# Kernel optimization log

Measured on AMD Instinct MI355X. Metric: run time of the kernel, lower is better.

## Reference

```python
import jax, jax.numpy as jnp
import numpy as np

B, T, IN, H = 256, 512, 130, 512


def setup_inputs() -> dict:
    key = jax.random.key(0)
    ks = jax.random.split(key, 6)
    scale = 1.0 / np.sqrt(H)
    inputs = jax.random.normal(ks[0], (B, T, IN), dtype=jnp.float32)
    inputs_len = jax.random.randint(ks[1], (B,), 1, T + 1)
    h0 = jnp.zeros((B, H), dtype=jnp.float32)
    c0 = jnp.zeros((B, H), dtype=jnp.float32)
    W_ih = jax.random.normal(ks[2], (4 * H, IN - 2), dtype=jnp.float32) * scale
    W_hh = jax.random.normal(ks[3], (4 * H, H), dtype=jnp.float32) * scale
    b_ih = jax.random.normal(ks[4], (4 * H,), dtype=jnp.float32) * scale
    b_hh = jax.random.normal(ks[5], (4 * H,), dtype=jnp.float32) * scale
    return {"inputs": inputs, "inputs_len": inputs_len, "h0": h0, "c0": c0,
            "W_ih": W_ih, "W_hh": W_hh, "b_ih": b_ih, "b_hh": b_hh}


def reference(inputs, inputs_len, h0, c0, W_ih, W_hh, b_ih, b_hh):
    # stard_LSTM=True: drop last 2 input features (spatial coords)
    xs = jnp.transpose(inputs[:, :, :-2], (1, 0, 2))  # [T, B, IN-2]

    def step(carry, x_t):
        h, c = carry
        gates = x_t @ W_ih.T + b_ih + h @ W_hh.T + b_hh  # [B, 4H]
        i, f, g, o = jnp.split(gates, 4, axis=-1)  # torch LSTMCell gate order
        i = jax.nn.sigmoid(i)
        f = jax.nn.sigmoid(f)
        g = jnp.tanh(g)
        o = jax.nn.sigmoid(o)
        c = f * c + i * g
        h = o * jnp.tanh(c)
        return (h, c), h

    _, hs = jax.lax.scan(step, (h0, c0), xs)  # hs: [T, B, H]
    # gather last valid hidden state per sequence (outputs[len-1][b])
    batch_idx = jnp.arange(inputs.shape[0])
    return hs[inputs_len - 1, batch_idx]  # [B, H]
```

## Files before the change

### kernel.cpp

```cpp
#include <hip/hip_runtime.h>
#include <hip/hip_bf16.h>
#include <stdint.h>


#define NB 256
#define NT 512
#define NF 130
#define NK 128
#define NH 512

typedef float f32x4 __attribute__((ext_vector_type(4)));
typedef float f32x2 __attribute__((ext_vector_type(2)));
typedef short bf16x8 __attribute__((ext_vector_type(8)));

__device__ __forceinline__ short bf1(float f) {
  union { float f; uint32_t u; } v; v.f = f;
  uint32_t r = (v.u + 0x7FFFu + ((v.u >> 16) & 1u)) >> 16;
  return (short)r;
}

__device__ __forceinline__ bf16x8 cvt8(const float* p) {
  bf16x8 r;
#pragma unroll
  for (int i = 0; i < 4; ++i) {
    f32x2 t = *(const f32x2*)(p + 2 * i);
    r[2 * i]     = bf1(t[0]);
    r[2 * i + 1] = bf1(t[1]);
  }
  return r;
}

__device__ __forceinline__ float fsig(float x) {
  return __builtin_amdgcn_rcpf(1.0f + __builtin_amdgcn_exp2f(-1.44269504f * x));
}
__device__ __forceinline__ float ftanh(float x) {
  return 2.0f * __builtin_amdgcn_rcpf(1.0f + __builtin_amdgcn_exp2f(-2.88539008f * x)) - 1.0f;
}

__global__ __launch_bounds__(256, 1) void lstm_pers(
    const float* __restrict__ xin, const int* __restrict__ lens,
    const float* __restrict__ h0, const float* __restrict__ c0,
    const float* __restrict__ Wih, const float* __restrict__ Whh,
    const float* __restrict__ bih, const float* __restrict__ bhh,
    float* __restrict__ out, unsigned* __restrict__ cnt,
    unsigned short* __restrict__ hbuf ) {
  const int blk = blockIdx.x;
  const int g  = blk & 15;
  const int s  = blk >> 4;
  const int tid = threadIdx.x;
  const int w  = tid >> 6;
  const int l  = tid & 63;
  const int q  = l >> 4;
  const int col = l & 15;
  const int bidx = (g << 4) + col;
  const int qh = (l & 15) >> 2;
  const int sg = l & 3;
  const int hbase = (s << 5) + (w << 3);

  bf16x8 whh[2][16];
  bf16x8 wih[2][4];
#pragma unroll
  for (int m = 0; m < 2; ++m) {
    const int grow = sg * NH + hbase + (m << 2) + qh;
    const float* pw = Whh + (size_t)grow * NH + q * 8;
#pragma unroll
    for (int kt = 0; kt < 16; ++kt) whh[m][kt] = cvt8(pw + kt * 32);
    const float* pi = Wih + (size_t)grow * NK + q * 8;
#pragma unroll
    for (int kt = 0; kt < 4; ++kt) wih[m][kt] = cvt8(pi + kt * 32);
  }

  f32x4 bias[2];
  float cst[2];
  const int blen = lens[bidx];
#pragma unroll
  for (int m = 0; m < 2; ++m) {
    const int hid = hbase + (m << 2) + q;
#pragma unroll
    for (int p = 0; p < 4; ++p)
      bias[m][p] = bih[p * NH + hid] + bhh[p * NH + hid];
    cst[m] = c0[(size_t)bidx * NH + hid];
    __hip_atomic_store(&hbuf[(size_t)bidx * NH + hid],
                       (unsigned short)bf1(h0[(size_t)bidx * NH + hid]),
                       __ATOMIC_RELAXED, __HIP_MEMORY_SCOPE_AGENT);
  }

  asm volatile("s_waitcnt vmcnt(0)" ::: "memory");
  if (l == 0)
    __hip_atomic_fetch_add(cnt + g * 32, 1u, __ATOMIC_RELAXED, __HIP_MEMORY_SCOPE_AGENT);

  f32x2 xr[16];
  {
    const float* px = xin + (size_t)bidx * (NT * NF) + q * 8;
#pragma unroll
    for (int kt = 0; kt < 4; ++kt)
#pragma unroll
      for (int i = 0; i < 4; ++i)
        xr[kt * 4 + i] = *(const f32x2*)(px + kt * 32 + i * 2);
  }

  const unsigned short* hsb = hbuf + (size_t)bidx * NH + q * 8;
  unsigned short* hwb = hbuf + (size_t)bidx * NH;
  int dead = 0;

  for (int t = 0; t < NT; ++t) {
    f32x4 acc[2];
    acc[0] = bias[0];
    acc[1] = bias[1];
#pragma unroll
    for (int kt = 0; kt < 4; ++kt) {
      bf16x8 xf;
#pragma unroll
      for (int i = 0; i < 4; ++i) {
        xf[2 * i]     = bf1(xr[kt * 4 + i][0]);
        xf[2 * i + 1] = bf1(xr[kt * 4 + i][1]);
      }
#pragma unroll
      for (int m = 0; m < 2; ++m)
        acc[m] = __builtin_amdgcn_mfma_f32_16x16x32_bf16(wih[m][kt], xf, acc[m], 0, 0, 0);
    }
    if (l == 0 && !dead) {
      const unsigned tgt = 64u * (unsigned)(t + 1);
      long spins = 0;
      while (__hip_atomic_load(cnt + g * 32, __ATOMIC_RELAXED, __HIP_MEMORY_SCOPE_AGENT) < tgt) {
        __builtin_amdgcn_s_sleep(1);
        if (++spins > (1L << 19)) { dead = 1; break; }
      }
    }
    asm volatile("" ::: "memory");
    const unsigned short* hs = hsb + ((size_t)(t & 1)) * (NB * NH);
    union U { unsigned long long u[2]; bf16x8 v; };
    U hu[16];
#pragma unroll
    for (int kt = 0; kt < 16; ++kt) {
      hu[kt].u[0] = __hip_atomic_load((const unsigned long long*)(hs + kt * 32),
                                      __ATOMIC_RELAXED, __HIP_MEMORY_SCOPE_AGENT);
      hu[kt].u[1] = __hip_atomic_load((const unsigned long long*)(hs + kt * 32 + 4),
                                      __ATOMIC_RELAXED, __HIP_MEMORY_SCOPE_AGENT);
    }
#pragma unroll
    for (int kt = 0; kt < 16; ++kt)
#pragma unroll
      for (int m = 0; m < 2; ++m)
        acc[m] = __builtin_amdgcn_mfma_f32_16x16x32_bf16(whh[m][kt], hu[kt].v, acc[m], 0, 0, 0);
    unsigned short* hw = hwb + ((size_t)((t + 1) & 1)) * (NB * NH);
#pragma unroll
    for (int m = 0; m < 2; ++m) {
      const int hid = hbase + (m << 2) + q;
      float ig = fsig(acc[m][0]);
      float fg = fsig(acc[m][1]);
      float gg = ftanh(acc[m][2]);
      float og = fsig(acc[m][3]);
      float cc = fg * cst[m] + ig * gg;
      cst[m] = cc;
      float hh = og * ftanh(cc);
      __hip_atomic_store(&hw[hid], (unsigned short)bf1(hh),
                         __ATOMIC_RELAXED, __HIP_MEMORY_SCOPE_AGENT);
      if (t == blen - 1) out[(size_t)bidx * NH + hid] = hh;
    }
    asm volatile("s_waitcnt vmcnt(0)" ::: "memory");
    if (l == 0)
      __hip_atomic_fetch_add(cnt + g * 32, 1u, __ATOMIC_RELAXED, __HIP_MEMORY_SCOPE_AGENT);
    if (t + 1 < NT) {
      const float* px = xin + (size_t)bidx * (NT * NF) + (size_t)(t + 1) * NF + q * 8;
#pragma unroll
      for (int kt = 0; kt < 4; ++kt)
#pragma unroll
        for (int i = 0; i < 4; ++i)
          xr[kt * 4 + i] = *(const f32x2*)(px + kt * 32 + i * 2);
    }
  }
}

extern "C" void kernel_launch(void* const* d_in, const int* in_sizes, int n_in,
                              void* d_out, int out_size, void* d_ws, size_t ws_size,
                              hipStream_t stream) {
  const float* xin  = (const float*)d_in[0];
  const int*   lens = (const int*)d_in[1];
  const float* h0   = (const float*)d_in[2];
  const float* c0   = (const float*)d_in[3];
  const float* Wih  = (const float*)d_in[4];
  const float* Whh  = (const float*)d_in[5];
  const float* bih  = (const float*)d_in[6];
  const float* bhh  = (const float*)d_in[7];
  float* out = (float*)d_out;

  unsigned* cnt = (unsigned*)d_ws;
  unsigned short* hbuf = (unsigned short*)((char*)d_ws + 4096);

  hipMemsetAsync(d_ws, 0, 4096, stream);
  lstm_pers<<<dim3(256), dim3(256), 0, stream>>>(xin, lens, h0, c0, Wih, Whh, bih, bhh,
                                                 out, cnt, hbuf);
}
```

Baseline: 3.070 ms.

## Replace shared atomic counter with per-wave flag slots and pack hidden-state stores

The single contended fetch-add counter per batch group becomes 64 per-wave slots, each set by exchange to the next timestep. Every lane polls one slot and a wave ballot decides readiness, which removes atomic contention on one address. Hidden-state bf16 values are gathered across lanes with ds_bpermute and written as 64-bit stores instead of many 16-bit stores. The x prefetch for the next step is moved ahead of the MFMAs, and the recurrent MFMA chain is split into two accumulators to shorten the dependency chain. In exchange there are more polling loads per step and extra cross-lane shuffles.

```diff
diff --git a/kernel.cpp b/kernel.cpp
--- a/kernel.cpp
+++ b/kernel.cpp
@@ -13,10 +13,9 @@
 typedef float f32x2 __attribute__((ext_vector_type(2)));
 typedef short bf16x8 __attribute__((ext_vector_type(8)));
 
-__device__ __forceinline__ short bf1(float f) {
+__device__ __forceinline__ unsigned bf1(float f) {
   union { float f; uint32_t u; } v; v.f = f;
-  uint32_t r = (v.u + 0x7FFFu + ((v.u >> 16) & 1u)) >> 16;
-  return (short)r;
+  return (v.u + 0x7FFFu + ((v.u >> 16) & 1u)) >> 16;
 }
 
 __device__ __forceinline__ bf16x8 cvt8(const float* p) {
@@ -24,8 +23,8 @@
 #pragma unroll
   for (int i = 0; i < 4; ++i) {
     f32x2 t = *(const f32x2*)(p + 2 * i);
-    r[2 * i]     = bf1(t[0]);
-    r[2 * i + 1] = bf1(t[1]);
+    r[2 * i]     = (short)bf1(t[0]);
+    r[2 * i + 1] = (short)bf1(t[1]);
   }
   return r;
 }
@@ -42,7 +41,7 @@
     const float* __restrict__ h0, const float* __restrict__ c0,
     const float* __restrict__ Wih, const float* __restrict__ Whh,
     const float* __restrict__ bih, const float* __restrict__ bhh,
-    float* __restrict__ out, unsigned* __restrict__ cnt,
+    float* __restrict__ out, unsigned* __restrict__ slots,
     unsigned short* __restrict__ hbuf ) {
   const int blk = blockIdx.x;
   const int g  = blk & 15;
@@ -56,6 +55,8 @@
   const int qh = (l & 15) >> 2;
   const int sg = l & 3;
   const int hbase = (s << 5) + (w << 3);
+  const int wid = (s << 2) + w;
+  unsigned* slot = slots + g * 64;
 
   bf16x8 whh[2][16];
   bf16x8 wih[2][4];
@@ -80,51 +81,87 @@
     for (int p = 0; p < 4; ++p)
       bias[m][p] = bih[p * NH + hid] + bhh[p * NH + hid];
     cst[m] = c0[(size_t)bidx * NH + hid];
-    __hip_atomic_store(&hbuf[(size_t)bidx * NH + hid],
-                       (unsigned short)bf1(h0[(size_t)bidx * NH + hid]),
-                       __ATOMIC_RELAXED, __HIP_MEMORY_SCOPE_AGENT);
-  }
-
+  }
+
+#define PUBLISH(val32, hw)                                                        \
+  {                                                                               \
+    unsigned pv0 = __builtin_amdgcn_ds_bpermute((col + 0) * 4, (int)(val32));     \
+    unsigned pv1 = __builtin_amdgcn_ds_bpermute((col + 16) * 4, (int)(val32));    \
+    unsigned pv2 = __builtin_amdgcn_ds_bpermute((col + 32) * 4, (int)(val32));    \
+    unsigned pv3 = __builtin_amdgcn_ds_bpermute((col + 48) * 4, (int)(val32));    \
+    if (l < 32) {                                                                 \
+      unsigned lo, hi;                                                            \
+      if (q == 0) { lo = (pv0 & 0xFFFFu) | (pv1 << 16);                           \
+                    hi = (pv2 & 0xFFFFu) | (pv3 << 16); }                         \
+      else        { lo = (pv0 >> 16) | (pv1 & 0xFFFF0000u);                       \
+                    hi = (pv2 >> 16) | (pv3 & 0xFFFF0000u); }                     \
+      unsigned long long pk = ((unsigned long long)hi << 32) | lo;                \
+      unsigned long long* dst =                                                   \
+          (unsigned long long*)((hw) + hbase + (q ? 4 : 0));                      \
+      (void)__hip_atomic_exchange(dst, pk, __ATOMIC_RELAXED,                      \
+                                  __HIP_MEMORY_SCOPE_AGENT);                      \
+    }                                                                             \
+  }
+
+  {
+    unsigned b0 = bf1(h0[(size_t)bidx * NH + hbase + 0 + q]);
+    unsigned b1 = bf1(h0[(size_t)bidx * NH + hbase + 4 + q]);
+    unsigned val32 = b0 | (b1 << 16);
+    unsigned short* hw = hbuf + (size_t)bidx * NH;
+    PUBLISH(val32, hw);
+  }
   asm volatile("s_waitcnt vmcnt(0)" ::: "memory");
   if (l == 0)
-    __hip_atomic_fetch_add(cnt + g * 32, 1u, __ATOMIC_RELAXED, __HIP_MEMORY_SCOPE_AGENT);
-
+    (void)__hip_atomic_exchange(slot + wid, 1u, __ATOMIC_RELAXED,
+                                __HIP_MEMORY_SCOPE_AGENT);
+
+  const float* px0 = xin + (size_t)bidx * (NT * NF) + q * 8;
   f32x2 xr[16];
-  {
-    const float* px = xin + (size_t)bidx * (NT * NF) + q * 8;
-#pragma unroll
-    for (int kt = 0; kt < 4; ++kt)
-#pragma unroll
-      for (int i = 0; i < 4; ++i)
-        xr[kt * 4 + i] = *(const f32x2*)(px + kt * 32 + i * 2);
-  }
+#pragma unroll
+  for (int kt = 0; kt < 4; ++kt)
+#pragma unroll
+    for (int i = 0; i < 4; ++i)
+      xr[kt * 4 + i] = *(const f32x2*)(px0 + kt * 32 + i * 2);
 
   const unsigned short* hsb = hbuf + (size_t)bidx * NH + q * 8;
   unsigned short* hwb = hbuf + (size_t)bidx * NH;
   int dead = 0;
 
   for (int t = 0; t < NT; ++t) {
-    f32x4 acc[2];
-    acc[0] = bias[0];
-    acc[1] = bias[1];
-#pragma unroll
-    for (int kt = 0; kt < 4; ++kt) {
-      bf16x8 xf;
+    bf16x8 xf[4];
+#pragma unroll
+    for (int kt = 0; kt < 4; ++kt)
 #pragma unroll
       for (int i = 0; i < 4; ++i) {
-        xf[2 * i]     = bf1(xr[kt * 4 + i][0]);
-        xf[2 * i + 1] = bf1(xr[kt * 4 + i][1]);
+        xf[kt][2 * i]     = (short)bf1(xr[kt * 4 + i][0]);
+        xf[kt][2 * i + 1] = (short)bf1(xr[kt * 4 + i][1]);
       }
+    {
+      const int tp = (t + 1 < NT) ? t + 1 : NT - 1;
+      const float* px = px0 + (size_t)tp * NF;
+#pragma unroll
+      for (int kt = 0; kt < 4; ++kt)
+#pragma unroll
+        for (int i = 0; i < 4; ++i)
+          xr[kt * 4 + i] = *(const f32x2*)(px + kt * 32 + i * 2);
+    }
+    f32x4 accA[2], accB[2];
+    accA[0] = bias[0]; accA[1] = bias[1];
+    accB[0] = (f32x4){0.f, 0.f, 0.f, 0.f}; accB[1] = accB[0];
+#pragma unroll
+    for (int kt = 0; kt < 4; ++kt)
 #pragma unroll
       for (int m = 0; m < 2; ++m)
-        acc[m] = __builtin_amdgcn_mfma_f32_16x16x32_bf16(wih[m][kt], xf, acc[m], 0, 0, 0);
-    }
-    if (l == 0 && !dead) {
-      const unsigned tgt = 64u * (unsigned)(t + 1);
-      long spins = 0;
-      while (__hip_atomic_load(cnt + g * 32, __ATOMIC_RELAXED, __HIP_MEMORY_SCOPE_AGENT) < tgt) {
+        accA[m] = __builtin_amdgcn_mfma_f32_16x16x32_bf16(wih[m][kt], xf[kt], accA[m], 0, 0, 0);
+    if (!dead) {
+      const unsigned tgt = (unsigned)(t + 1);
+      int iters = 0;
+      for (;;) {
+        unsigned sv = __hip_atomic_load(slot + l, __ATOMIC_RELAXED,
+                                        __HIP_MEMORY_SCOPE_AGENT);
+        if (__ballot(sv < tgt) == 0ULL) break;
         __builtin_amdgcn_s_sleep(1);
-        if (++spins > (1L << 19)) { dead = 1; break; }
+        if (++iters > (1 << 17)) { dead = 1; break; }
       }
     }
     asm volatile("" ::: "memory");
@@ -139,36 +176,38 @@
                                       __ATOMIC_RELAXED, __HIP_MEMORY_SCOPE_AGENT);
     }
 #pragma unroll
-    for (int kt = 0; kt < 16; ++kt)
-#pragma unroll
-      for (int m = 0; m < 2; ++m)
-        acc[m] = __builtin_amdgcn_mfma_f32_16x16x32_bf16(whh[m][kt], hu[kt].v, acc[m], 0, 0, 0);
+    for (int kt = 0; kt < 16; ++kt) {
+#pragma unroll
+      for (int m = 0; m < 2; ++m) {
+        if (kt & 1)
+          accB[m] = __builtin_amdgcn_mfma_f32_16x16x32_bf16(whh[m][kt], hu[kt].v, accB[m], 0, 0, 0);
+        else
+          accA[m] = __builtin_amdgcn_mfma_f32_16x16x32_bf16(whh[m][kt], hu[kt].v, accA[m], 0, 0, 0);
+      }
+    }
     unsigned short* hw = hwb + ((size_t)((t + 1) & 1)) * (NB * NH);
+    unsigned hbits[2];
 #pragma unroll
     for (int m = 0; m < 2; ++m) {
-      const int hid = hbase + (m << 2) + q;
-      float ig = fsig(acc[m][0]);
-      float fg = fsig(acc[m][1]);
-      float gg = ftanh(acc[m][2]);
-      float og = fsig(acc[m][3]);
+      f32x4 gv = accA[m] + accB[m];
+      float ig = fsig(gv[0]);
+      float fg = fsig(gv[1]);
+      float gg = ftanh(gv[2]);
+      float og = fsig(gv[3]);
       float cc = fg * cst[m] + ig * gg;
       cst[m] = cc;
       float hh = og * ftanh(cc);
-      __hip_atomic_store(&hw[hid], (unsigned short)bf1(hh),
-                         __ATOMIC_RELAXED, __HIP_MEMORY_SCOPE_AGENT);
-      if (t == blen - 1) out[(size_t)bidx * NH + hid] = hh;
+      hbits[m] = bf1(hh);
+      if (t == blen - 1) out[(size_t)bidx * NH + hbase + (m << 2) + q] = hh;
+    }
+    {
+      unsigned val32 = hbits[0] | (hbits[1] << 16);
+      PUBLISH(val32, hw);
     }
     asm volatile("s_waitcnt vmcnt(0)" ::: "memory");
     if (l == 0)
-      __hip_atomic_fetch_add(cnt + g * 32, 1u, __ATOMIC_RELAXED, __HIP_MEMORY_SCOPE_AGENT);
-    if (t + 1 < NT) {
-      const float* px = xin + (size_t)bidx * (NT * NF) + (size_t)(t + 1) * NF + q * 8;
-#pragma unroll
-      for (int kt = 0; kt < 4; ++kt)
-#pragma unroll
-        for (int i = 0; i < 4; ++i)
-          xr[kt * 4 + i] = *(const f32x2*)(px + kt * 32 + i * 2);
-    }
+      (void)__hip_atomic_exchange(slot + wid, (unsigned)(t + 2),
+                                  __ATOMIC_RELAXED, __HIP_MEMORY_SCOPE_AGENT);
   }
 }
 
@@ -185,10 +224,10 @@
   const float* bhh  = (const float*)d_in[7];
   float* out = (float*)d_out;
 
-  unsigned* cnt = (unsigned*)d_ws;
+  unsigned* slots = (unsigned*)d_ws;
   unsigned short* hbuf = (unsigned short*)((char*)d_ws + 4096);
 
   hipMemsetAsync(d_ws, 0, 4096, stream);
   lstm_pers<<<dim3(256), dim3(256), 0, stream>>>(xin, lens, h0, c0, Wih, Whh, bih, bhh,
-                                                 out, cnt, hbuf);
-}
+                                                 out, slots, hbuf);
+}
```

Result: slower. 4.082 ms (+32.9%).
